# Kernel tuning notes

Hardware: AMD Instinct MI355X
Metric: run time of the kernel (lower is better)

## Reference

```python
import jax, jax.numpy as jnp
import numpy as np

E, D_MODEL, D_FF = 8, 1024, 4096
B, S = 4, 2048


def setup_inputs() -> dict:
    key = jax.random.key(0)
    ks = jax.random.split(key, 7)
    scale_in = 1.0 / np.sqrt(D_MODEL)
    scale_ff = 1.0 / np.sqrt(D_FF)
    return {
        "x": jax.random.normal(ks[0], (B, S, D_MODEL), dtype=jnp.float32),
        "w1": jax.random.normal(ks[1], (E, D_MODEL, D_FF), dtype=jnp.float32) * scale_in,
        "b1": jax.random.normal(ks[2], (E, D_FF), dtype=jnp.float32) * 0.01,
        "w2": jax.random.normal(ks[3], (E, D_FF, D_MODEL), dtype=jnp.float32) * scale_ff,
        "b2": jax.random.normal(ks[4], (E, D_MODEL), dtype=jnp.float32) * 0.01,
        "gate_w": jax.random.normal(ks[5], (D_MODEL, E), dtype=jnp.float32) * scale_in,
        "gate_b": jax.random.normal(ks[6], (E,), dtype=jnp.float32) * 0.01,
    }


def reference(x, w1, b1, w2, b2, gate_w, gate_b):
    # Gating: softmax then top-1 (argmax of probs == argmax of logits)
    gate_logits = x @ gate_w + gate_b                      # [B,S,E]
    gate_probs = jax.nn.softmax(gate_logits, axis=-1)
    top1 = jnp.argmax(gate_probs, axis=-1)                 # [B,S] int
    mask = jax.nn.one_hot(top1, E, dtype=x.dtype)          # [B,S,E]

    # Dense compute of every expert on every token (faithful to source)
    h = jax.nn.relu(jnp.einsum('bsd,edf->ebsf', x, w1) + b1[:, None, None, :])  # [E,B,S,F]
    y = jnp.einsum('ebsf,efd->ebsd', h, w2) + b2[:, None, None, :]              # [E,B,S,D]

    # Top-1 mask-and-sum combine (note: no gate-prob scaling in the original)
    out = jnp.einsum('ebsd,bse->bsd', y, mask)             # [B,S,D]
    return out
```

## Files before the change

### kernel.cpp

```cpp
#include <hip/hip_runtime.h>
#include <stdint.h>

#define DM 1024
#define DF 4096
#define NE 8
#define NTOK 8192
#define MT_LAUNCH 72

typedef __attribute__((ext_vector_type(8))) short short8;
typedef __attribute__((ext_vector_type(8))) unsigned short ushort8v;
typedef __attribute__((ext_vector_type(4))) float floatx4;

__device__ inline unsigned short f2bf(float f) {
    union { float f; unsigned u; } v; v.f = f;
    unsigned u = v.u;
    u += 0x7fffu + ((u >> 16) & 1u);
    return (unsigned short)(u >> 16);
}

#define GLDS(g, l) __builtin_amdgcn_global_load_lds( \
    (const __attribute__((address_space(1))) void*)(g), \
    (__attribute__((address_space(3))) void*)(l), 16, 0, 0)

__global__ void gate_kernel(const float* __restrict__ x, const float* __restrict__ gw,
                            const float* __restrict__ gb, int* __restrict__ top1) {
    int t = blockIdx.x;
    int lane = threadIdx.x;
    const float* xr = x + (size_t)t * DM;
    double acc[NE];
#pragma unroll
    for (int e = 0; e < NE; ++e) acc[e] = 0.0;
    for (int j = 0; j < DM / 64; ++j) {
        int d = j * 64 + lane;
        double xv = (double)xr[d];
        const float* g = gw + (size_t)d * NE;
#pragma unroll
        for (int e = 0; e < NE; ++e) acc[e] = fma(xv, (double)g[e], acc[e]);
    }
#pragma unroll
    for (int e = 0; e < NE; ++e) {
        for (int off = 32; off > 0; off >>= 1)
            acc[e] += __shfl_down(acc[e], off, 64);
    }
    if (lane == 0) {
        int best = 0;
        double bv = acc[0] + (double)gb[0];
        for (int e = 1; e < NE; ++e) {
            double v = acc[e] + (double)gb[e];
            if (v > bv) { bv = v; best = e; }
        }
        top1[t] = best;
    }
}

__global__ void count_kernel(const int* __restrict__ top1, int* __restrict__ ctrl) {
    int t = blockIdx.x * 256 + threadIdx.x;
    int e = top1[t];
    int lane = threadIdx.x & 63;
#pragma unroll
    for (int ex = 0; ex < NE; ++ex) {
        unsigned long long m = __ballot(e == ex);
        if (m != 0ull && lane == (__ffsll((long long)m) - 1))
            atomicAdd(&ctrl[ex], __popcll(m));
    }
}

__global__ void prefix_kernel(int* ctrl) {
    if (threadIdx.x == 0) {
        int s = 0, t = 0;
        for (int e = 0; e < NE; ++e) {
            int cnt = ctrl[e];
            ctrl[8 + e] = s; ctrl[17 + e] = s;
            for (int m = 0; m * 128 < cnt; ++m) {
                ctrl[32 + 3 * t] = e;
                ctrl[33 + 3 * t] = s + m * 128;
                int rr = cnt - m * 128;
                ctrl[34 + 3 * t] = rr < 128 ? rr : 128;
                ++t;
            }
            s += cnt;
        }
        ctrl[16] = s;
        ctrl[25] = t;
    }
}

__global__ void scatter_kernel(const int* __restrict__ top1, int* __restrict__ ctrl,
                               int* __restrict__ perm) {
    int t = blockIdx.x * 256 + threadIdx.x;
    int e = top1[t];
    int lane = threadIdx.x & 63;
#pragma unroll
    for (int ex = 0; ex < NE; ++ex) {
        unsigned long long m = __ballot(e == ex);
        if (m == 0ull) continue;
        int leader = __ffsll((long long)m) - 1;
        int base = 0;
        if (lane == leader) base = atomicAdd(&ctrl[17 + ex], __popcll(m));
        base = __shfl(base, leader, 64);
        if (e == ex) {
            int pos = __popcll(m & ((1ull << lane) - 1ull));
            perm[base + pos] = t;
        }
    }
}

__global__ void convert_x(const float* __restrict__ x, unsigned short* __restrict__ xb) {
    int i = blockIdx.x * 256 + threadIdx.x;
    const float4* x4 = (const float4*)x;
    float4 v = x4[i];
    ushort4 o;
    o.x = f2bf(v.x); o.y = f2bf(v.y); o.z = f2bf(v.z); o.w = f2bf(v.w);
    ((ushort4*)xb)[i] = o;
}

__global__ void transpose_bf16(const float* __restrict__ src, unsigned short* __restrict__ dst,
                               int R, int C) {
    __shared__ float tile[64][65];
    int tilesR = R >> 6, tilesC = C >> 6;
    int bid = blockIdx.x;
    int e = bid / (tilesR * tilesC);
    int rem = bid % (tilesR * tilesC);
    int tr = rem / tilesC, tc = rem % tilesC;
    const float* s = src + (size_t)e * R * C + (size_t)(tr * 64) * C + tc * 64;
    unsigned short* d = dst + (size_t)e * R * C + (size_t)(tc * 64) * R + tr * 64;
    int tid = threadIdx.x;
#pragma unroll
    for (int i = 0; i < 4; ++i) {
        int idx = i * 256 + tid;
        int r = idx >> 4, c4 = (idx & 15) * 4;
        float4 v = *(const float4*)(s + (size_t)r * C + c4);
        tile[r][c4 + 0] = v.x; tile[r][c4 + 1] = v.y;
        tile[r][c4 + 2] = v.z; tile[r][c4 + 3] = v.w;
    }
    __syncthreads();
#pragma unroll
    for (int i = 0; i < 2; ++i) {
        int idx = i * 256 + tid;
        int c = idx >> 3, r8 = (idx & 7) * 8;
        ushort8v o;
#pragma unroll
        for (int j = 0; j < 8; ++j) o[j] = f2bf(tile[r8 + j][c]);
        *(ushort8v*)(d + (size_t)c * R + r8) = o;
    }
}

template<bool FFN1>
__global__ __launch_bounds__(256) void ffn_gemm(
    const unsigned short* __restrict__ A,
    const unsigned short* __restrict__ Bt,
    const float* __restrict__ bias,
    const int* __restrict__ ctrl,
    const int* __restrict__ perm,
    unsigned short* __restrict__ Hout,
    float* __restrict__ Yout) {
    constexpr int K  = FFN1 ? DM : DF;
    constexpr int N  = FFN1 ? DF : DM;
    constexpr int KS = FFN1 ? 1 : 2;
    constexpr int KLEN = K / KS;
    constexpr int NT = N / 128;
    constexpr int G = 8;
    constexpr int INNER = NT * KS;

    int b = blockIdx.x;
    int grp = b / (G * INNER);
    int ii = b % (G * INNER);
    int til = grp * G + ii / INNER;
    int r2 = ii % INNER;
    int nt = r2 / KS;
    int ksp = r2 % KS;
    if (til >= ctrl[25]) return;
    int e       = ctrl[32 + 3 * til];
    int rowbase = ctrl[33 + 3 * til];
    int rows    = ctrl[34 + 3 * til];

    __shared__ __align__(16) unsigned short As[128 * 64];
    __shared__ __align__(16) unsigned short Bs[128 * 64];

    int tid = threadIdx.x;
    int lane = tid & 63;
    int wave = tid >> 6;
    int wm = (wave & 1) * 64;
    int wn = (wave >> 1) * 64;

    const unsigned short* arow[4];
    const unsigned short* brow[4];
    const unsigned short* bbase = Bt + (size_t)e * N * K + (size_t)(nt * 128) * K;
#pragma unroll
    for (int i = 0; i < 4; ++i) {
        int c = i * 256 + tid;
        int r = c >> 3;
        int gk = (c & 7) ^ (r & 7);
        int rr = r < rows ? r : rows - 1;
        int cr = rowbase + rr;
        int srow = FFN1 ? perm[cr] : cr;
        arow[i] = A + (size_t)srow * K + gk * 8;
        brow[i] = bbase + (size_t)r * K + gk * 8;
    }

    floatx4 acc[4][4];
#pragma unroll
    for (int i = 0; i < 4; ++i)
#pragma unroll
        for (int j = 0; j < 4; ++j) acc[i][j] = floatx4{0.f, 0.f, 0.f, 0.f};

    for (int kk = ksp * KLEN; kk < ksp * KLEN + KLEN; kk += 64) {
#pragma unroll
        for (int i = 0; i < 4; ++i) {
            GLDS(arow[i] + kk, &As[(i * 256 + tid) * 8]);
            GLDS(brow[i] + kk, &Bs[(i * 256 + tid) * 8]);
        }
        __syncthreads();
#pragma unroll
        for (int ks = 0; ks < 2; ++ks) {
            short8 af[4], bfr[4];
#pragma unroll
            for (int m = 0; m < 4; ++m) {
                int R = wm + m * 16 + (lane & 15);
                int s = (ks * 4 + (lane >> 4)) ^ (R & 7);
                af[m] = *(const short8*)&As[R * 64 + s * 8];
            }
#pragma unroll
            for (int n = 0; n < 4; ++n) {
                int R = wn + n * 16 + (lane & 15);
                int s = (ks * 4 + (lane >> 4)) ^ (R & 7);
                bfr[n] = *(const short8*)&Bs[R * 64 + s * 8];
            }
#pragma unroll
            for (int m = 0; m < 4; ++m)
#pragma unroll
                for (int n = 0; n < 4; ++n)
                    acc[m][n] = __builtin_amdgcn_mfma_f32_16x16x32_bf16(af[m], bfr[n], acc[m][n], 0, 0, 0);
        }
        __syncthreads();
    }

    int col0 = nt * 128 + wn + (lane & 15);
    int rowq = (lane >> 4) * 4;
    float bv[4];
#pragma unroll
    for (int n = 0; n < 4; ++n) bv[n] = (FFN1 || ksp == 0) ? bias[e * N + col0 + n * 16] : 0.f;

#pragma unroll
    for (int m = 0; m < 4; ++m) {
#pragma unroll
        for (int r = 0; r < 4; ++r) {
            int lr = wm + m * 16 + rowq + r;
            if (lr < rows) {
                if (FFN1) {
                    unsigned short* hr = Hout + (size_t)(rowbase + lr) * DF + col0;
#pragma unroll
                    for (int n = 0; n < 4; ++n) {
                        float v = acc[m][n][r] + bv[n];
                        v = v > 0.f ? v : 0.f;
                        hr[n * 16] = f2bf(v);
                    }
                } else {
                    float* yr = Yout + (size_t)perm[rowbase + lr] * DM + col0;
#pragma unroll
                    for (int n = 0; n < 4; ++n)
                        atomicAdd(&yr[n * 16], acc[m][n][r] + bv[n]);
                }
            }
        }
    }
}

extern "C" void kernel_launch(void* const* d_in, const int* in_sizes, int n_in,
                              void* d_out, int out_size, void* d_ws, size_t ws_size,
                              hipStream_t stream) {
    const float* x  = (const float*)d_in[0];
    const float* w1 = (const float*)d_in[1];
    const float* b1 = (const float*)d_in[2];
    const float* w2 = (const float*)d_in[3];
    const float* b2 = (const float*)d_in[4];
    const float* gw = (const float*)d_in[5];
    const float* gb = (const float*)d_in[6];
    float* out = (float*)d_out;

    char* ws = (char*)d_ws;
    int* ctrl = (int*)ws;
    int* top1 = (int*)(ws + 1024);
    int* perm = (int*)(ws + 1024 + 32768);
    size_t o = 66560;
    unsigned short* xb  = (unsigned short*)(ws + o);        o += (size_t)NTOK * DM * 2;
    unsigned short* w1t = (unsigned short*)(ws + o);        o += (size_t)NE * DM * DF * 2;
    unsigned short* w2t = (unsigned short*)(ws + o);        o += (size_t)NE * DM * DF * 2;
    unsigned short* H   = (unsigned short*)(ws + o);

    hipMemsetAsync(ctrl, 0, 1024, stream);
    hipMemsetAsync(out, 0, (size_t)out_size * 4, stream);
    gate_kernel<<<NTOK, 64, 0, stream>>>(x, gw, gb, top1);
    count_kernel<<<NTOK / 256, 256, 0, stream>>>(top1, ctrl);
    prefix_kernel<<<1, 64, 0, stream>>>(ctrl);
    scatter_kernel<<<NTOK / 256, 256, 0, stream>>>(top1, ctrl, perm);
    convert_x<<<NTOK * DM / 4 / 256, 256, 0, stream>>>(x, xb);
    transpose_bf16<<<NE * (DM / 64) * (DF / 64), 256, 0, stream>>>(w1, w1t, DM, DF);
    transpose_bf16<<<NE * (DF / 64) * (DM / 64), 256, 0, stream>>>(w2, w2t, DF, DM);
    ffn_gemm<true ><<<MT_LAUNCH * (DF / 128), 256, 0, stream>>>(xb, w1t, b1, ctrl, perm, H, nullptr);
    ffn_gemm<false><<<MT_LAUNCH * (DM / 128) * 2, 256, 0, stream>>>(H, w2t, b2, ctrl, perm, nullptr, out);
}
```

Baseline: 680.7 us.

## Double-buffer GEMM LDS tiles, remap blocks per XCD, fuse bf16 convert into gate

The expert GEMM kernel now double-buffers its LDS tiles, issuing the next K-slice's global-to-LDS loads before computing the current one so memory latency overlaps MFMA work. Block indices are remapped so consecutive logical tiles land on the same XCD, and the tile ordering now puts the N-tile outermost, which is meant to improve L2 reuse of weight and activation tiles. The separate x-to-bf16 conversion kernel is folded into the gate kernel, removing one launch and one extra read of x. Doubling LDS to 64KB per block may lower occupancy, and the gate kernel now does scalar 2-byte stores.

Measured after the change: 645.4 us. 1.05x faster.

```diff
diff --git a/kernel.cpp b/kernel.cpp
--- a/kernel.cpp
+++ b/kernel.cpp
@@ -23,16 +23,20 @@
     (__attribute__((address_space(3))) void*)(l), 16, 0, 0)
 
 __global__ void gate_kernel(const float* __restrict__ x, const float* __restrict__ gw,
-                            const float* __restrict__ gb, int* __restrict__ top1) {
+                            const float* __restrict__ gb, int* __restrict__ top1,
+                            unsigned short* __restrict__ xb) {
     int t = blockIdx.x;
     int lane = threadIdx.x;
     const float* xr = x + (size_t)t * DM;
+    unsigned short* xbr = xb + (size_t)t * DM;
     double acc[NE];
 #pragma unroll
     for (int e = 0; e < NE; ++e) acc[e] = 0.0;
     for (int j = 0; j < DM / 64; ++j) {
         int d = j * 64 + lane;
-        double xv = (double)xr[d];
+        float xf = xr[d];
+        xbr[d] = f2bf(xf);
+        double xv = (double)xf;
         const float* g = gw + (size_t)d * NE;
 #pragma unroll
         for (int e = 0; e < NE; ++e) acc[e] = fma(xv, (double)g[e], acc[e]);
@@ -105,15 +109,6 @@
     }
 }
 
-__global__ void convert_x(const float* __restrict__ x, unsigned short* __restrict__ xb) {
-    int i = blockIdx.x * 256 + threadIdx.x;
-    const float4* x4 = (const float4*)x;
-    float4 v = x4[i];
-    ushort4 o;
-    o.x = f2bf(v.x); o.y = f2bf(v.y); o.z = f2bf(v.z); o.w = f2bf(v.w);
-    ((ushort4*)xb)[i] = o;
-}
-
 __global__ void transpose_bf16(const float* __restrict__ src, unsigned short* __restrict__ dst,
                                int R, int C) {
     __shared__ float tile[64][65];
@@ -144,6 +139,36 @@
         *(ushort8v*)(d + (size_t)c * R + r8) = o;
     }
 }
+
+#define STAGE(BUF, KK) do { \
+    _Pragma("unroll") \
+    for (int i_ = 0; i_ < 4; ++i_) { \
+        GLDS(arow[i_] + (KK), &As[BUF][(i_ * 256 + tid) * 8]); \
+        GLDS(brow[i_] + (KK), &Bs[BUF][(i_ * 256 + tid) * 8]); \
+    } } while (0)
+
+#define COMPUTE(BUF) do { \
+    _Pragma("unroll") \
+    for (int ks_ = 0; ks_ < 2; ++ks_) { \
+        short8 af[4], bfr[4]; \
+        _Pragma("unroll") \
+        for (int m_ = 0; m_ < 4; ++m_) { \
+            int R_ = wm + m_ * 16 + (lane & 15); \
+            int s_ = (ks_ * 4 + (lane >> 4)) ^ (R_ & 7); \
+            af[m_] = *(const short8*)&As[BUF][R_ * 64 + s_ * 8]; \
+        } \
+        _Pragma("unroll") \
+        for (int n_ = 0; n_ < 4; ++n_) { \
+            int R_ = wn + n_ * 16 + (lane & 15); \
+            int s_ = (ks_ * 4 + (lane >> 4)) ^ (R_ & 7); \
+            bfr[n_] = *(const short8*)&Bs[BUF][R_ * 64 + s_ * 8]; \
+        } \
+        _Pragma("unroll") \
+        for (int m_ = 0; m_ < 4; ++m_) \
+            _Pragma("unroll") \
+            for (int n_ = 0; n_ < 4; ++n_) \
+                acc[m_][n_] = __builtin_amdgcn_mfma_f32_16x16x32_bf16(af[m_], bfr[n_], acc[m_][n_], 0, 0, 0); \
+    } } while (0)
 
 template<bool FFN1>
 __global__ __launch_bounds__(256) void ffn_gemm(
@@ -161,21 +186,27 @@
     constexpr int NT = N / 128;
     constexpr int G = 8;
     constexpr int INNER = NT * KS;
-
-    int b = blockIdx.x;
+    constexpr int NKI = KLEN / 64;
+
+    int nwg = gridDim.x;
+    int bo = blockIdx.x;
+    int q = nwg >> 3, r = nwg & 7;
+    int xcd = bo & 7, lid = bo >> 3;
+    int b = (xcd < r ? xcd * (q + 1) : r * (q + 1) + (xcd - r) * q) + lid;
+
     int grp = b / (G * INNER);
     int ii = b % (G * INNER);
-    int til = grp * G + ii / INNER;
-    int r2 = ii % INNER;
-    int nt = r2 / KS;
-    int ksp = r2 % KS;
+    int nt  = ii / (G * KS);
+    int rem = ii % (G * KS);
+    int til = grp * G + rem / KS;
+    int ksp = rem % KS;
     if (til >= ctrl[25]) return;
     int e       = ctrl[32 + 3 * til];
     int rowbase = ctrl[33 + 3 * til];
     int rows    = ctrl[34 + 3 * til];
 
-    __shared__ __align__(16) unsigned short As[128 * 64];
-    __shared__ __align__(16) unsigned short Bs[128 * 64];
+    __shared__ __align__(16) unsigned short As[2][128 * 64];
+    __shared__ __align__(16) unsigned short Bs[2][128 * 64];
 
     int tid = threadIdx.x;
     int lane = tid & 63;
@@ -189,13 +220,13 @@
 #pragma unroll
     for (int i = 0; i < 4; ++i) {
         int c = i * 256 + tid;
-        int r = c >> 3;
-        int gk = (c & 7) ^ (r & 7);
-        int rr = r < rows ? r : rows - 1;
+        int rr2 = c >> 3;
+        int gk = (c & 7) ^ (rr2 & 7);
+        int rr = rr2 < rows ? rr2 : rows - 1;
         int cr = rowbase + rr;
         int srow = FFN1 ? perm[cr] : cr;
         arow[i] = A + (size_t)srow * K + gk * 8;
-        brow[i] = bbase + (size_t)r * K + gk * 8;
+        brow[i] = bbase + (size_t)rr2 * K + gk * 8;
     }
 
     floatx4 acc[4][4];
@@ -204,34 +235,18 @@
 #pragma unroll
         for (int j = 0; j < 4; ++j) acc[i][j] = floatx4{0.f, 0.f, 0.f, 0.f};
 
-    for (int kk = ksp * KLEN; kk < ksp * KLEN + KLEN; kk += 64) {
-#pragma unroll
-        for (int i = 0; i < 4; ++i) {
-            GLDS(arow[i] + kk, &As[(i * 256 + tid) * 8]);
-            GLDS(brow[i] + kk, &Bs[(i * 256 + tid) * 8]);
-        }
+    int kk0 = ksp * KLEN;
+
+    STAGE(0, kk0);
+    __syncthreads();
+#pragma unroll 1
+    for (int t = 0; t < NKI; t += 2) {
+        int kk = kk0 + t * 64;
+        STAGE(1, kk + 64);
+        COMPUTE(0);
         __syncthreads();
-#pragma unroll
-        for (int ks = 0; ks < 2; ++ks) {
-            short8 af[4], bfr[4];
-#pragma unroll
-            for (int m = 0; m < 4; ++m) {
-                int R = wm + m * 16 + (lane & 15);
-                int s = (ks * 4 + (lane >> 4)) ^ (R & 7);
-                af[m] = *(const short8*)&As[R * 64 + s * 8];
-            }
-#pragma unroll
-            for (int n = 0; n < 4; ++n) {
-                int R = wn + n * 16 + (lane & 15);
-                int s = (ks * 4 + (lane >> 4)) ^ (R & 7);
-                bfr[n] = *(const short8*)&Bs[R * 64 + s * 8];
-            }
-#pragma unroll
-            for (int m = 0; m < 4; ++m)
-#pragma unroll
-                for (int n = 0; n < 4; ++n)
-                    acc[m][n] = __builtin_amdgcn_mfma_f32_16x16x32_bf16(af[m], bfr[n], acc[m][n], 0, 0, 0);
-        }
+        if (t + 2 < NKI) STAGE(0, kk + 128);
+        COMPUTE(1);
         __syncthreads();
     }
 
@@ -244,14 +259,14 @@
 #pragma unroll
     for (int m = 0; m < 4; ++m) {
 #pragma unroll
-        for (int r = 0; r < 4; ++r) {
-            int lr = wm + m * 16 + rowq + r;
+        for (int r2 = 0; r2 < 4; ++r2) {
+            int lr = wm + m * 16 + rowq + r2;
             if (lr < rows) {
                 if (FFN1) {
                     unsigned short* hr = Hout + (size_t)(rowbase + lr) * DF + col0;
 #pragma unroll
                     for (int n = 0; n < 4; ++n) {
-                        float v = acc[m][n][r] + bv[n];
+                        float v = acc[m][n][r2] + bv[n];
                         v = v > 0.f ? v : 0.f;
                         hr[n * 16] = f2bf(v);
                     }
@@ -259,12 +274,15 @@
                     float* yr = Yout + (size_t)perm[rowbase + lr] * DM + col0;
 #pragma unroll
                     for (int n = 0; n < 4; ++n)
-                        atomicAdd(&yr[n * 16], acc[m][n][r] + bv[n]);
+                        atomicAdd(&yr[n * 16], acc[m][n][r2] + bv[n]);
                 }
             }
         }
     }
 }
+
+#undef STAGE
+#undef COMPUTE
 
 extern "C" void kernel_launch(void* const* d_in, const int* in_sizes, int n_in,
                               void* d_out, int out_size, void* d_ws, size_t ws_size,
@@ -290,11 +308,10 @@
 
     hipMemsetAsync(ctrl, 0, 1024, stream);
     hipMemsetAsync(out, 0, (size_t)out_size * 4, stream);
-    gate_kernel<<<NTOK, 64, 0, stream>>>(x, gw, gb, top1);
+    gate_kernel<<<NTOK, 64, 0, stream>>>(x, gw, gb, top1, xb);
     count_kernel<<<NTOK / 256, 256, 0, stream>>>(top1, ctrl);
     prefix_kernel<<<1, 64, 0, stream>>>(ctrl);
     scatter_kernel<<<NTOK / 256, 256, 0, stream>>>(top1, ctrl, perm);
-    convert_x<<<NTOK * DM / 4 / 256, 256, 0, stream>>>(x, xb);
     transpose_bf16<<<NE * (DM / 64) * (DF / 64), 256, 0, stream>>>(w1, w1t, DM, DF);
     transpose_bf16<<<NE * (DF / 64) * (DM / 64), 256, 0, stream>>>(w2, w2t, DF, DM);
     ffn_gemm<true ><<<MT_LAUNCH * (DF / 128), 256, 0, stream>>>(xb, w1t, b1, ctrl, perm, H, nullptr);
```
